# Kernel tuning notes

Hardware: AMD Instinct MI355X
Metric: run time of the kernel (lower is better)

Reference implementation:

```python
import jax, jax.numpy as jnp
import numpy as np

K = 9
HF = WF = 128
SAMPLING = 16
H_IMG = W_IMG = 2048.0
ANC_RATIO = np.array([0.5, 1.0, 2.0])
ANC_SIZE = np.array([8.0, 16.0, 32.0])
TOPN_NMS = 6000
N_NMS = 2000
THR_NMS = 0.7


def generate_anchors():
    # loop order in original GenerateAnchor: ii over Wf (ctrx), jj over Hf (ctry), ratio, size
    ctrx = (np.arange(WF) + 0.5) * SAMPLING  # [Wf]
    ctry = (np.arange(HF) + 0.5) * SAMPLING  # [Hf]
    w = SAMPLING * ANC_SIZE[None, :] / np.sqrt(ANC_RATIO)[:, None]  # [R,S]
    h = SAMPLING * ANC_SIZE[None, :] * np.sqrt(ANC_RATIO)[:, None]
    cx = ctrx[:, None, None, None]  # [Wf,1,1,1]
    cy = ctry[None, :, None, None]  # [1,Hf,1,1]
    w = w[None, None]; h = h[None, None]  # [1,1,R,S]
    x1, y1 = cx - w / 2, cy - h / 2
    x2, y2 = cx + w / 2, cy + h / 2
    anc = np.stack(np.broadcast_arrays(x1, y1, x2, y2), axis=-1).reshape(-1, 4)
    return np.round(anc).astype(np.float32)  # [Wf*Hf*K, 4]


def conv2d(x, w, b, pad):
    y = jax.lax.conv_general_dilated(
        x, w, (1, 1), [(pad, pad), (pad, pad)],
        dimension_numbers=('NCHW', 'OIHW', 'NCHW'))
    return y + b[None, :, None, None]


def pairwise_iou(b):
    # Faithful to my_IoU: 'gt' (pivot, row i) coords are int-truncated;
    # intersection via min(all)+w_a+w_g-max(all); union uses raw/truncated areas.
    ax1, ay1, ax2, ay2 = b[:, 0], b[:, 1], b[:, 2], b[:, 3]
    aw, ah = ax2 - ax1, ay2 - ay1
    aminx, amaxx = jnp.minimum(ax1, ax2), jnp.maximum(ax1, ax2)
    aminy, amaxy = jnp.minimum(ay1, ay2), jnp.maximum(ay1, ay2)
    tx1, ty1, tx2, ty2 = jnp.trunc(ax1), jnp.trunc(ay1), jnp.trunc(ax2), jnp.trunc(ay2)
    gminx, gmaxx = jnp.minimum(tx1, tx2), jnp.maximum(tx1, tx2)
    gminy, gmaxy = jnp.minimum(ty1, ty2), jnp.maximum(ty1, ty2)
    gw, gh = jnp.trunc(ax2 - ax1), jnp.trunc(ay2 - ay1)
    iw = jnp.maximum(jnp.minimum(aminx[None, :], gminx[:, None]) + aw[None, :]
                     + gw[:, None] - jnp.maximum(amaxx[None, :], gmaxx[:, None]), 0.0)
    ih = jnp.maximum(jnp.minimum(aminy[None, :], gminy[:, None]) + ah[None, :]
                     + gh[:, None] - jnp.maximum(amaxy[None, :], gmaxy[:, None]), 0.0)
    inter = iw * ih  # [i=pivot, j=candidate]
    union = (aw * ah)[None, :] + (gw * gh)[:, None] - inter
    return inter / union


def make_roi(anchor, delta, obj):
    # delta2xy
    aw = anchor[:, 2] - anchor[:, 0]
    ah = anchor[:, 3] - anchor[:, 1]
    acx = anchor[:, 0] + aw / 2
    acy = anchor[:, 1] + ah / 2
    cx = delta[:, 0] * aw + acx
    cy = delta[:, 1] * ah + acy
    w = jnp.exp(delta[:, 2]) * aw
    h = jnp.exp(delta[:, 3]) * ah
    roi = jnp.stack([cx - w / 2, cy - h / 2, cx + w / 2, cy + h / 2], axis=1)
    # clip exactly as original: negatives->0; >H -> H-1; >W -> W-1
    roi = jnp.maximum(roi, 0.0)
    roi = roi.at[:, 3].set(jnp.where(roi[:, 3] > H_IMG, H_IMG - 1.0, roi[:, 3]))
    roi = roi.at[:, 2].set(jnp.where(roi[:, 2] > W_IMG, W_IMG - 1.0, roi[:, 2]))
    valid = (roi[:, 2] - roi[:, 0] > SAMPLING) & (roi[:, 3] - roi[:, 1] > SAMPLING)
    scores = jnp.where(valid, obj, -jnp.inf)  # mask instead of dropping (jit-friendly)
    top_scores, top_idx = jax.lax.top_k(scores, TOPN_NMS)
    boxes = roi[top_idx]
    keep0 = jnp.isfinite(top_scores)
    iou = pairwise_iou(boxes)  # [TOPN, TOPN]
    idxs = jnp.arange(TOPN_NMS)

    def body(i, keep):
        sup = keep[i] & (iou[i] >= THR_NMS) & (idxs > i)
        return keep & ~sup

    keep = jax.lax.fori_loop(0, TOPN_NMS, body, keep0)
    rank = jnp.cumsum(keep) - 1
    pos = jnp.where(keep & (rank < N_NMS), rank, N_NMS)  # out-of-range rows dropped
    out = jnp.zeros((N_NMS, 4), boxes.dtype).at[pos].set(boxes, mode='drop')
    return out


def setup_inputs() -> dict:
    key = jax.random.key(0)
    ks = jax.random.split(key, 4)
    featmap = jax.random.normal(ks[0], (1, 512, HF, WF), dtype=jnp.float32)
    conv3_w = jax.random.normal(ks[1], (512, 512, 3, 3), dtype=jnp.float32) * 0.01
    conv3_b = jnp.zeros((512,), jnp.float32)
    cls_w = jax.random.normal(ks[2], (2 * K, 512, 1, 1), dtype=jnp.float32) * 0.01
    cls_b = jnp.zeros((2 * K,), jnp.float32)
    reg_w = jax.random.normal(ks[3], (4 * K, 512, 1, 1), dtype=jnp.float32) * 0.01
    reg_b = jnp.zeros((4 * K,), jnp.float32)
    return {'featmap': featmap, 'conv3_w': conv3_w, 'conv3_b': conv3_b,
            'cls_w': cls_w, 'cls_b': cls_b, 'reg_w': reg_w, 'reg_b': reg_b}


def reference(featmap, conv3_w, conv3_b, cls_w, cls_b, reg_w, reg_b):
    x = jax.nn.relu(conv2d(featmap, conv3_w, conv3_b, 1))
    pred_cls = conv2d(x, cls_w, cls_b, 0)  # [1, 2k, Hf, Wf]
    pred_reg = conv2d(x, reg_w, reg_b, 0)  # [1, 4k, Hf, Wf]
    pred_cls = jnp.transpose(pred_cls, (0, 2, 3, 1)).reshape(1, -1, 2)
    pred_reg = jnp.transpose(pred_reg, (0, 2, 3, 1)).reshape(1, -1, 4)
    pred_obj = pred_cls[:, :, 1]
    anchors = jnp.asarray(generate_anchors())
    # roi path is detached in the original (uses .data)
    roi = make_roi(anchors,
                   jax.lax.stop_gradient(pred_reg[0]),
                   jax.lax.stop_gradient(pred_obj[0]))
    return roi, pred_cls, pred_reg
```

## Files before the change

kernel.cpp:

```cpp
#include <hip/hip_runtime.h>

#define HF 128
#define WF 128
#define KANC 9
#define NANC (HF*WF*KANC)
#define NSORT 262144
#define TOPN 6000
#define NWORDS 94
#define NOUT 2000
#define OFF_CLS 8000
#define OFF_REG 302912
#define NCAND 8192
#define NBCAP 2048

typedef unsigned long long u64;
typedef double d4 __attribute__((ext_vector_type(4)));
typedef const __attribute__((address_space(1))) void* gas1;
typedef __attribute__((address_space(3))) void* las3;

__global__ __launch_bounds__(256) void zero3_k(double* p1, int n1,
                                               double* p2, int n2,
                                               unsigned* hist, u64* selp,
                                               unsigned* cnt) {
  int i = blockIdx.x * 256 + threadIdx.x;
  if (i < n1) p1[i] = 0.0;
  else if (i - n1 < n2) p2[i - n1] = 0.0;
  if (i < 2048) hist[i] = 0;
  if (i == 0) { selp[0] = 0; selp[1] = 0; cnt[0] = 0; cnt[1] = 0; }
}

__global__ __launch_bounds__(256) void wtrans_k(const float* __restrict__ w,
                                                float* __restrict__ wt) {
  __shared__ float ld[64 * 73];
  int t = threadIdx.x;
  int ocg = blockIdx.x & 7, icg = blockIdx.x >> 3;
  int oc0 = ocg << 6, ic0 = icg << 3;
  #pragma unroll
  for (int rep = 0; rep < 18; ++rep) {
    int idx = rep * 256 + t;
    int row = idx / 72, col = idx - row * 72;
    ld[row * 73 + col] = w[(size_t)(oc0 + row) * 4608 + ic0 * 9 + col];
  }
  __syncthreads();
  #pragma unroll
  for (int rep = 0; rep < 18; ++rep) {
    int idx = rep * 256 + t;
    int pair = idx >> 6, oc = idx & 63;
    int tap = pair % 9, ic = pair / 9;
    wt[(size_t)tap * 262144 + (size_t)(ic0 + ic) * 512 + oc0 + oc] =
        ld[oc * 73 + ic * 9 + tap];
  }
}

#define BKC 32
#define NCHUNK 144

__global__ __launch_bounds__(256, 4) void conv_mfma_k(
    const float* __restrict__ feat, const float* __restrict__ wt,
    const float* __restrict__ conv_b, const float* __restrict__ cls_w,
    const float* __restrict__ reg_w, double* __restrict__ predacc)
{
  __shared__ __align__(16) char smraw[32768];
  float* AsB = (float*)smraw;
  float* BsB = (float*)(smraw + 2 * 2048 * 4);
  int tid = threadIdx.x;
  int bid = blockIdx.x;
  int pt = bid & 255, ot = bid >> 8;
  int h = pt >> 1, w0 = (pt & 1) << 6;
  int oc0 = ot << 6;
  int wv = tid >> 6, l = tid & 63;
  int wr = wv >> 1, wc = wv & 1;
  int lg = l >> 4, lr = l & 15;

  d4 acc[2][2];
  #pragma unroll
  for (int t = 0; t < 2; ++t)
    #pragma unroll
    for (int u = 0; u < 2; ++u) acc[t][u] = (d4)0.0;

  float4 areg[2];

  auto gloadA = [&](int c) {
    int tap = c >> 4, ic0 = (c & 15) << 5;
    int kh = tap / 3 - 1, kw = tap % 3 - 1;
    int hp = h + kh;
    bool okh = ((unsigned)hp < 128u);
    #pragma unroll
    for (int i = 0; i < 2; ++i) {
      int q = tid + (i << 8);
      int r = q >> 4, c0 = (q & 15) << 2;
      float v0 = 0.f, v1 = 0.f, v2 = 0.f, v3 = 0.f;
      const float* src = &feat[((ic0 + r) << 14) + (hp << 7)];
      int wp = w0 + c0 + kw;
      if (okh) {
        if ((unsigned)(wp + 0) < 128u) v0 = src[wp + 0];
        if ((unsigned)(wp + 1) < 128u) v1 = src[wp + 1];
        if ((unsigned)(wp + 2) < 128u) v2 = src[wp + 2];
        if ((unsigned)(wp + 3) < 128u) v3 = src[wp + 3];
      }
      areg[i] = make_float4(v0, v1, v2, v3);
    }
  };
  auto gloadB_lds = [&](int c, int buf) {
    float* B = BsB + buf * 2048;
    #pragma unroll
    for (int i = 0; i < 2; ++i) {
      int q = tid + (i << 8);
      int r = q >> 4, c0 = (q & 15) << 2;
      const float* src =
          &wt[(size_t)((c << 5) + r) * 512 + oc0 + (c0 ^ ((r & 1) << 4))];
      __builtin_amdgcn_global_load_lds((gas1)src, (las3)&B[q << 2], 16, 0, 0);
    }
  };
  auto dswriteA = [&](int buf) {
    float* A = AsB + buf * 2048;
    #pragma unroll
    for (int i = 0; i < 2; ++i) {
      int q = tid + (i << 8);
      int r = q >> 4, c0 = (q & 15) << 2;
      *(float4*)&A[(r << 6) + (c0 ^ ((r & 1) << 4))] = areg[i];
    }
  };
  auto compute = [&](int buf) {
    const float* A = AsB + buf * 2048;
    const float* B = BsB + buf * 2048;
    #pragma unroll
    for (int k4 = 0; k4 < BKC; k4 += 4) {
      int krow = k4 + lg;
      int sw = (krow & 1) << 4;
      double a0 = (double)A[(krow << 6) + (((wr << 5) + lr) ^ sw)];
      double a1 = (double)A[(krow << 6) + (((wr << 5) + 16 + lr) ^ sw)];
      double b0 = (double)B[(krow << 6) + (((wc << 5) + lr) ^ sw)];
      double b1 = (double)B[(krow << 6) + (((wc << 5) + 16 + lr) ^ sw)];
      acc[0][0] = __builtin_amdgcn_mfma_f64_16x16x4f64(a0, b0, acc[0][0], 0, 0, 0);
      acc[0][1] = __builtin_amdgcn_mfma_f64_16x16x4f64(a0, b1, acc[0][1], 0, 0, 0);
      acc[1][0] = __builtin_amdgcn_mfma_f64_16x16x4f64(a1, b0, acc[1][0], 0, 0, 0);
      acc[1][1] = __builtin_amdgcn_mfma_f64_16x16x4f64(a1, b1, acc[1][1], 0, 0, 0);
    }
  };

  gloadA(0);
  gloadB_lds(0, 0);
  dswriteA(0);
  for (int c = 0; c < NCHUNK; ++c) {
    __syncthreads();
    if (c + 1 < NCHUNK) {
      gloadB_lds(c + 1, (c + 1) & 1);
      gloadA(c + 1);
    }
    compute(c & 1);
    if (c + 1 < NCHUNK) dswriteA((c + 1) & 1);
  }

  int rmap[4], cmap[4];
  {
    d4 z = (d4)0.0;
    double apr = (lg == 0) ? (double)lr : 0.0;
    double bpr = (lg == 0) ? 1.0 : 0.0;
    d4 dr = __builtin_amdgcn_mfma_f64_16x16x4f64(apr, bpr, z, 0, 0, 0);
    double apc = (lg == 0) ? 1.0 : 0.0;
    double bpc = (lg == 0) ? (double)lr : 0.0;
    d4 dc = __builtin_amdgcn_mfma_f64_16x16x4f64(apc, bpc, z, 0, 0, 0);
    #pragma unroll
    for (int r = 0; r < 4; ++r) { rmap[r] = (int)dr[r]; cmap[r] = (int)dc[r]; }
  }

  double* xs = (double*)smraw;
  float* hwS = (float*)(smraw + 32 * 65 * 8);
  __syncthreads();
  for (int e = tid; e < 54 * 64; e += 256) {
    int o = e >> 6, j = e & 63;
    hwS[e] = (o < 18) ? cls_w[(o << 9) + oc0 + j]
                      : reg_w[((o - 18) << 9) + oc0 + j];
  }
  int pixbase = (h << 7) + w0;
  #pragma unroll
  for (int ph = 0; ph < 2; ++ph) {
    if (wr == ph) {
      #pragma unroll
      for (int t = 0; t < 2; ++t) {
        #pragma unroll
        for (int u = 0; u < 2; ++u) {
          #pragma unroll
          for (int r = 0; r < 4; ++r) {
            int ocl = (wc << 5) + (u << 4) + cmap[r];
            int pxl = (t << 4) + rmap[r];
            double v = acc[t][u][r] + (double)conv_b[oc0 + ocl];
            xs[pxl * 65 + ocl] = (v > 0.0) ? v : 0.0;
          }
        }
      }
    }
    __syncthreads();
    #pragma unroll
    for (int it = 0; it < 7; ++it) {
      int e = tid + (it << 8);
      if (e < 54 * 32) {
        int o = e >> 5, px = e & 31;
        const double* xr = &xs[px * 65];
        const float* hr = &hwS[o << 6];
        double s = 0.0;
        #pragma unroll
        for (int j = 0; j < 64; ++j) s += xr[j] * (double)hr[j];
        atomicAdd(&predacc[(size_t)(pixbase + (ph << 5) + px) * 54 + o], s);
      }
    }
    __syncthreads();
  }
}

__global__ __launch_bounds__(256) void chk_x_k(
    const float* __restrict__ feat, const float* __restrict__ c3w,
    double* __restrict__ xraw)
{
  int task = blockIdx.x * 256 + threadIdx.x;
  int pi = task >> 14;
  int oc = (task >> 5) & 511;
  int icg = task & 31;
  const int pixs[4] = {0, 5437, 10240, 16383};
  int pix = pixs[pi];
  int h = pix >> 7, w = pix & 127;
  double s = 0.0;
  for (int ic = icg * 16; ic < icg * 16 + 16; ++ic) {
    const float* f = &feat[ic << 14];
    const float* wp = &c3w[(size_t)(oc * 512 + ic) * 9];
    #pragma unroll
    for (int kh = -1; kh <= 1; ++kh) {
      int hp = h + kh;
      if ((unsigned)hp >= 128u) continue;
      #pragma unroll
      for (int kw = -1; kw <= 1; ++kw) {
        int wq = w + kw;
        if ((unsigned)wq >= 128u) continue;
        s += (double)f[(hp << 7) + wq] * (double)wp[(kh + 1) * 3 + (kw + 1)];
      }
    }
  }
  atomicAdd(&xraw[(pi << 9) + oc], s);
}

__global__ __launch_bounds__(256) void chk_cmp_k(
    const double* __restrict__ xraw, const float* __restrict__ c3b,
    const float* __restrict__ cls_w, const float* __restrict__ reg_w,
    const double* __restrict__ predacc, double* flagd)
{
  int t = threadIdx.x;
  if (t >= 216) return;
  int pi = t / 54, o = t - pi * 54;
  const int pixs[4] = {0, 5437, 10240, 16383};
  const float* wrow = (o < 18) ? &cls_w[o << 9] : &reg_w[(o - 18) << 9];
  const double* xr = &xraw[pi << 9];
  double s = 0.0;
  for (int j = 0; j < 512; ++j) {
    double x = xr[j] + (double)c3b[j];
    x = x > 0.0 ? x : 0.0;
    s += x * (double)wrow[j];
  }
  double got = predacc[(size_t)pixs[pi] * 54 + o];
  if (fabs(got - s) > 1e-6) *flagd = 1.0;
}

__global__ __launch_bounds__(256) void rezero_k(const double* __restrict__ flagd,
                                                double* p, int n) {
  if (*flagd == 0.0) return;
  int i = blockIdx.x * 256 + threadIdx.x;
  if (i < n) p[i] = 0.0;
}

__global__ __launch_bounds__(256) void conv_fb_k(
    const double* __restrict__ flagd,
    const float* __restrict__ feat, const float* __restrict__ wt,
    const float* __restrict__ conv_b, const float* __restrict__ cls_w,
    const float* __restrict__ reg_w, double* __restrict__ predacc)
{
  if (*flagd == 0.0) return;
  __shared__ __align__(16) char smraw[47104];
  double* As = (double*)smraw;
  double* Bs = As + 2048;
  int tid = threadIdx.x;
  int bid = blockIdx.x;
  int pt = bid & 255, ot = bid >> 8;
  int h = pt >> 1, w0 = (pt & 1) << 6;
  int oc0 = ot << 6;
  int tx = tid & 15, ty = tid >> 4;

  double acc[4][4];
  #pragma unroll
  for (int i = 0; i < 4; ++i)
    #pragma unroll
    for (int j = 0; j < 4; ++j) acc[i][j] = 0.0;

  for (int tap = 0; tap < 9; ++tap) {
    int kh = tap / 3 - 1, kw = tap % 3 - 1;
    int hp = h + kh;
    bool okh = (hp >= 0) && (hp < HF);
    for (int icc = 0; icc < 16; ++icc) {
      int ic0 = icc << 5;
      __syncthreads();
      #pragma unroll
      for (int i = 0; i < 8; ++i) {
        int e = tid + (i << 8);
        int icl = e >> 6;
        int lx = e & 63;
        int wp = w0 + lx + kw;
        float v = 0.0f;
        if (okh && wp >= 0 && wp < WF)
          v = feat[((ic0 + icl) << 14) + (hp << 7) + wp];
        As[(icl << 6) + lx] = (double)v;
        Bs[(icl << 6) + lx] =
            (double)wt[((((tap << 9) + ic0 + icl)) << 9) + oc0 + lx];
      }
      __syncthreads();
      #pragma unroll
      for (int k = 0; k < 32; ++k) {
        const double* ar = &As[(k << 6) + (ty << 2)];
        const double* br = &Bs[(k << 6) + (tx << 2)];
        double a0 = ar[0], a1 = ar[1], a2 = ar[2], a3 = ar[3];
        double b0 = br[0], b1 = br[1], b2 = br[2], b3 = br[3];
        acc[0][0] += a0 * b0; acc[0][1] += a0 * b1; acc[0][2] += a0 * b2; acc[0][3] += a0 * b3;
        acc[1][0] += a1 * b0; acc[1][1] += a1 * b1; acc[1][2] += a1 * b2; acc[1][3] += a1 * b3;
        acc[2][0] += a2 * b0; acc[2][1] += a2 * b1; acc[2][2] += a2 * b2; acc[2][3] += a2 * b3;
        acc[3][0] += a3 * b0; acc[3][1] += a3 * b1; acc[3][2] += a3 * b2; acc[3][3] += a3 * b3;
      }
    }
  }
  __syncthreads();
  double* xs = (double*)smraw;
  float* hwS = (float*)(smraw + 64 * 65 * 8);
  #pragma unroll
  for (int i = 0; i < 4; ++i) {
    int px = (ty << 2) + i;
    #pragma unroll
    for (int j = 0; j < 4; ++j) {
      int oc = (tx << 2) + j;
      double v = acc[i][j] + (double)conv_b[oc0 + oc];
      xs[px * 65 + oc] = v > 0.0 ? v : 0.0;
    }
  }
  for (int e = tid; e < 54 * 64; e += 256) {
    int o = e >> 6, ocl = e & 63;
    hwS[e] = (o < 18) ? cls_w[(o << 9) + oc0 + ocl]
                      : reg_w[((o - 18) << 9) + oc0 + ocl];
  }
  __syncthreads();
  int pixbase = (h << 7) + w0;
  for (int e = tid; e < 54 * 64; e += 256) {
    int px = e & 63, o = e >> 6;
    const double* xr = &xs[px * 65];
    const float* hr = &hwS[o << 6];
    double s = 0.0;
    #pragma unroll
    for (int j = 0; j < 64; ++j) s += xr[j] * (double)hr[j];
    atomicAdd(&predacc[(pixbase + px) * 54 + o], s);
  }
}

__global__ __launch_bounds__(256) void anchor_k(
    const double* __restrict__ predacc, const float* __restrict__ cls_b,
    const float* __restrict__ reg_b, float* __restrict__ out,
    double* __restrict__ roi_all, double* __restrict__ scores_d,
    ulonglong2* __restrict__ sortb)
{
  #pragma clang fp contract(off)
  int a = blockIdx.x * 256 + threadIdx.x;
  if (a >= NSORT) return;
  if (a >= NANC) {
    sortb[a] = make_ulonglong2(0xFFF0000000000000ULL, 0xFFFFFFFFULL);
    return;
  }
  int pix = a / 9;
  int k = a - pix * 9;
  int h = pix >> 7, wq = pix & 127;
  const double* pa = &predacc[pix * 54];
  double c0 = pa[2 * k] + (double)cls_b[2 * k];
  double c1 = pa[2 * k + 1] + (double)cls_b[2 * k + 1];
  double d0 = pa[18 + 4 * k + 0] + (double)reg_b[4 * k + 0];
  double d1 = pa[18 + 4 * k + 1] + (double)reg_b[4 * k + 1];
  double d2 = pa[18 + 4 * k + 2] + (double)reg_b[4 * k + 2];
  double d3 = pa[18 + 4 * k + 3] + (double)reg_b[4 * k + 3];
  out[OFF_CLS + a * 2 + 0] = (float)c0;
  out[OFF_CLS + a * 2 + 1] = (float)c1;
  out[OFF_REG + a * 4 + 0] = (float)d0;
  out[OFF_REG + a * 4 + 1] = (float)d1;
  out[OFF_REG + a * 4 + 2] = (float)d2;
  out[OFF_REG + a * 4 + 3] = (float)d3;
  int ir = k / 3, is = k - ir * 3;
  double ratio = (ir == 0) ? 0.5 : (ir == 1 ? 1.0 : 2.0);
  double asz = (is == 0) ? 8.0 : (is == 1 ? 16.0 : 32.0);
  double sq = sqrt(ratio);
  double wa = (16.0 * asz) / sq;
  double ha = (16.0 * asz) * sq;
  double cx = (h + 0.5) * 16.0;
  double cy = (wq + 0.5) * 16.0;
  double A0 = (double)(float)rint(cx - wa * 0.5);
  double A1 = (double)(float)rint(cy - ha * 0.5);
  double A2 = (double)(float)rint(cx + wa * 0.5);
  double A3 = (double)(float)rint(cy + ha * 0.5);
  double aw = A2 - A0, ah = A3 - A1;
  double acx = A0 + aw * 0.5, acy = A1 + ah * 0.5;
  double ccx = d0 * aw + acx;
  double ccy = d1 * ah + acy;
  double wr = exp(d2) * aw;
  double hh = exp(d3) * ah;
  double r0 = ccx - wr * 0.5;
  double r1 = ccy - hh * 0.5;
  double r2 = ccx + wr * 0.5;
  double r3 = ccy + hh * 0.5;
  r0 = fmax(r0, 0.0); r1 = fmax(r1, 0.0); r2 = fmax(r2, 0.0); r3 = fmax(r3, 0.0);
  r3 = (r3 > 2048.0) ? 2047.0 : r3;
  r2 = (r2 > 2048.0) ? 2047.0 : r2;
  bool valid = ((r2 - r0) > 16.0) && ((r3 - r1) > 16.0);
  double score = valid ? c1 : -__builtin_huge_val();
  roi_all[a * 4 + 0] = r0;
  roi_all[a * 4 + 1] = r1;
  roi_all[a * 4 + 2] = r2;
  roi_all[a * 4 + 3] = r3;
  scores_d[a] = score;
  u64 u = (u64)__double_as_longlong(score);
  u64 m = (u >> 63) ? ~u : (u | 0x8000000000000000ULL);
  sortb[a] = make_ulonglong2(~m, (u64)a);
}

__global__ __launch_bounds__(1024) void hist_k(const ulonglong2* __restrict__ sortb,
                                               unsigned* __restrict__ hist,
                                               const u64* __restrict__ selp,
                                               int pass) {
  __shared__ unsigned h[2048];
  int t = threadIdx.x;
  h[t] = 0; h[t + 1024] = 0;
  __syncthreads();
  const int SH[3] = {53, 42, 31};
  const u64 PM[3] = {0ULL, 0xFFE0000000000000ULL, 0xFFFFFC0000000000ULL};
  u64 pfx = selp[0];
  u64 pm = PM[pass];
  int sh = SH[pass];
  for (int e = blockIdx.x * 1024 + t; e < NSORT; e += gridDim.x * 1024) {
    u64 k = sortb[e].x;
    if ((k & pm) == pfx)
      atomicAdd(&h[(unsigned)((k >> sh) & 2047)], 1u);
  }
  __syncthreads();
  if (h[t]) atomicAdd(&hist[t], h[t]);
  if (h[t + 1024]) atomicAdd(&hist[t + 1024], h[t + 1024]);
}

__global__ __launch_bounds__(1024) void scan_k(unsigned* hist, u64* selp, int pass) {
  __shared__ unsigned h[2048];
  int t = threadIdx.x;
  h[t] = hist[t]; h[t + 1024] = hist[t + 1024];
  hist[t] = 0; hist[t + 1024] = 0;
  __syncthreads();
  if (t == 0) {
    const int SH[3] = {53, 42, 31};
    u64 cum = selp[1];
    u64 pfx = selp[0];
    int b = 0;
    for (; b < 2047; ++b) {
      if (cum + h[b] >= (u64)TOPN) break;
      cum += h[b];
    }
    selp[0] = pfx | ((u64)b << SH[pass]);
    selp[1] = cum;
  }
}

__global__ __launch_bounds__(1024) void compact_k(
    const ulonglong2* __restrict__ sortb, const u64* __restrict__ selp,
    ulonglong2* __restrict__ cand, ulonglong2* __restrict__ bcand,
    unsigned* __restrict__ cnt) {
  u64 pfx = selp[0];
  const u64 M33 = 0xFFFFFFFF80000000ULL;
  for (int e = blockIdx.x * 1024 + threadIdx.x; e < NSORT; e += gridDim.x * 1024) {
    ulonglong2 v = sortb[e];
    u64 top = v.x & M33;
    if (top < pfx) {
      unsigned p = atomicAdd(&cnt[0], 1u);
      if (p < NCAND) cand[p] = v;
    } else if (top == pfx) {
      unsigned p = atomicAdd(&cnt[1], 1u);
      if (p < NBCAP) bcand[p] = v;
    }
  }
}

__device__ __forceinline__ bool sless(ulonglong2 A, ulonglong2 B) {
  return (A.x < B.x) || (A.x == B.x && A.y < B.y);
}

__global__ __launch_bounds__(1024) void sortprep_k(
    const ulonglong2* __restrict__ cand, const ulonglong2* __restrict__ bcand,
    const unsigned* __restrict__ cnt, const double* __restrict__ roi_all,
    const double* __restrict__ scores_d, double* __restrict__ boxes,
    u64* __restrict__ removed)
{
  extern __shared__ ulonglong2 s[];
  int t = threadIdx.x;
  unsigned ci = cnt[0]; if (ci > NCAND) ci = NCAND;
  unsigned cb = cnt[1]; if (cb > NBCAP) cb = NBCAP;
  #pragma unroll
  for (int i = 0; i < 8; ++i) {
    int p = t + (i << 10);
    ulonglong2 v;
    if (p < (int)ci) v = cand[p];
    else if (p < (int)(ci + cb)) v = bcand[p - ci];
    else v = make_ulonglong2(~0ULL, ~0ULL);
    s[p] = v;
  }
  __syncthreads();
  for (int k = 2; k <= NCAND; k <<= 1) {
    for (int j = k >> 1; j >= 1; j >>= 1) {
      #pragma unroll
      for (int q = 0; q < 4; ++q) {
        int p = t + (q << 10);
        int li = ((p & ~(j - 1)) << 1) | (p & (j - 1));
        int pa = li | j;
        bool asc = ((li & k) == 0);
        ulonglong2 A = s[li], B = s[pa];
        bool sw = asc ? sless(B, A) : sless(A, B);
        if (sw) { s[li] = B; s[pa] = A; }
      }
      __syncthreads();
    }
  }
  for (int i = t; i < TOPN; i += 1024) {
    unsigned idx = (unsigned)s[i].y;
    double b0 = 0, b1 = 0, b2 = 0, b3 = 0;
    if (idx < NANC) {
      b0 = roi_all[idx * 4 + 0];
      b1 = roi_all[idx * 4 + 1];
      b2 = roi_all[idx * 4 + 2];
      b3 = roi_all[idx * 4 + 3];
    }
    boxes[i * 4 + 0] = b0; boxes[i * 4 + 1] = b1;
    boxes[i * 4 + 2] = b2; boxes[i * 4 + 3] = b3;
  }
  if (t < NWORDS) {
    u64 wdd = (t == NWORDS - 1) ? 0xFFFF000000000000ULL : 0ULL;
    for (int b = 0; b < 64; ++b) {
      int i = t * 64 + b;
      if (i >= TOPN) break;
      unsigned idx = (unsigned)s[i].y;
      bool dead = true;
      if (idx < NANC) dead = isinf(scores_d[idx]);
      if (dead) wdd |= (1ULL << b);
    }
    removed[t] = wdd;
  }
}

__global__ __launch_bounds__(256) void mask_k(const double* __restrict__ boxes,
                                              u64* __restrict__ mask) {
  #pragma clang fp contract(off)
  int gw = (blockIdx.x * 256 + threadIdx.x) >> 6;
  int lane = threadIdx.x & 63;
  int i = gw / NWORDS, wj = gw - i * NWORDS;
  if (i >= TOPN) return;
  if (wj < (i >> 6)) return;
  double ix1 = boxes[i * 4 + 0], iy1 = boxes[i * 4 + 1];
  double ix2 = boxes[i * 4 + 2], iy2 = boxes[i * 4 + 3];
  double tx1 = trunc(ix1), ty1 = trunc(iy1), tx2 = trunc(ix2), ty2 = trunc(iy2);
  double gminx = fmin(tx1, tx2), gmaxx = fmax(tx1, tx2);
  double gminy = fmin(ty1, ty2), gmaxy = fmax(ty1, ty2);
  double gw_ = trunc(ix2 - ix1), gh_ = trunc(iy2 - iy1);
  int j = wj * 64 + lane;
  bool pred = false;
  if (j < TOPN && j > i) {
    double jx1 = boxes[j * 4 + 0], jy1 = boxes[j * 4 + 1];
    double jx2 = boxes[j * 4 + 2], jy2 = boxes[j * 4 + 3];
    double aw = jx2 - jx1, ah = jy2 - jy1;
    double aminx = fmin(jx1, jx2), amaxx = fmax(jx1, jx2);
    double aminy = fmin(jy1, jy2), amaxy = fmax(jy1, jy2);
    double iw = fmin(aminx, gminx) + aw + gw_ - fmax(amaxx, gmaxx);
    iw = fmax(iw, 0.0);
    double ih = fmin(aminy, gminy) + ah + gh_ - fmax(amaxy, gmaxy);
    ih = fmax(ih, 0.0);
    double inter = iw * ih;
    double uni = aw * ah + gw_ * gh_ - inter;
    pred = (inter / uni >= 0.7);
  }
  u64 bal = __ballot(pred);
  if (lane == 0) mask[(size_t)i * NWORDS + wj] = bal;
}

__global__ __launch_bounds__(1024) void nms_chunk_k(const u64* __restrict__ mask,
                                                    u64* removed_g) {
  __shared__ u64 rem[NWORDS];
  __shared__ u64 aliveSh;
  int t = threadIdx.x;
  int lane = t & 63;
  int wvid = t >> 6;
  if (t < NWORDS) rem[t] = removed_g[t];
  __syncthreads();
  for (int c = 0; c < NWORDS; ++c) {
    if (wvid == 0) {
      int i = c * 64 + lane;
      u64 diag = (i < TOPN) ? mask[(size_t)i * NWORDS + c] : 0ULL;
      u64 local = rem[c];
      #pragma unroll 1
      for (int j = 0; j < 64; ++j) {
        u64 dj = __shfl(diag, j);
        if (!((local >> j) & 1ULL)) local |= dj;
      }
      if (lane == 0) { rem[c] = local; aliveSh = ~local; }
    }
    __syncthreads();
    u64 alive = aliveSh;
    int nw = NWORDS - 1 - c;
    if (nw > 0 && alive) {
      int npairs = 64 * nw;
      for (int p = t; p < npairs; p += 1024) {
        int j = p / nw;
        int w = c + 1 + (p - j * nw);
        if ((alive >> j) & 1ULL) {
          int i = c * 64 + j;
          if (i < TOPN) {
            u64 v = mask[(size_t)i * NWORDS + w];
            if (v) atomicOr(&rem[w], v);
          }
        }
      }
    }
    __syncthreads();
  }
  if (t < NWORDS) removed_g[t] = rem[t];
}

__global__ __launch_bounds__(256) void out_k(const u64* __restrict__ removed,
                                             const double* __restrict__ boxes,
                                             float* __restrict__ out) {
  __shared__ int pref[NWORDS + 1];
  __shared__ u64 keepw[NWORDS];
  int t = threadIdx.x;
  for (int i = t; i < NOUT * 4; i += 256) out[i] = 0.0f;
  if (t < NWORDS) keepw[t] = ~removed[t];
  __syncthreads();
  if (t == 0) {
    int s = 0;
    for (int w = 0; w < NWORDS; ++w) { pref[w] = s; s += __popcll(keepw[w]); }
    pref[NWORDS] = s;
  }
  __syncthreads();
  for (int i = t; i < TOPN; i += 256) {
    u64 kw = keepw[i >> 6];
    if ((kw >> (i & 63)) & 1ULL) {
      int rank = pref[i >> 6] + __popcll(kw & ((1ULL << (i & 63)) - 1ULL));
      if (rank < NOUT) {
        out[rank * 4 + 0] = (float)boxes[i * 4 + 0];
        out[rank * 4 + 1] = (float)boxes[i * 4 + 1];
        out[rank * 4 + 2] = (float)boxes[i * 4 + 2];
        out[rank * 4 + 3] = (float)boxes[i * 4 + 3];
      }
    }
  }
}

extern "C" void kernel_launch(void* const* d_in, const int* in_sizes, int n_in,
                              void* d_out, int out_size, void* d_ws, size_t ws_size,
                              hipStream_t stream) {
  const float* feat = (const float*)d_in[0];
  const float* c3w = (const float*)d_in[1];
  const float* c3b = (const float*)d_in[2];
  const float* clw = (const float*)d_in[3];
  const float* clb = (const float*)d_in[4];
  const float* rgw = (const float*)d_in[5];
  const float* rgb = (const float*)d_in[6];
  float* out = (float*)d_out;
  char* ws = (char*)d_ws;
  size_t off = 0;
  auto alloc = [&](size_t bytes) {
    size_t o = off;
    off = (off + bytes + 255) & ~(size_t)255;
    return o;
  };
  double* predacc = (double*)(ws + alloc(16384ULL * 54 * 8));
  double* flagd = (double*)(ws + alloc(256));
  float* wt = (float*)(ws + alloc(2359296ULL * 4));
  double* roi_all = (double*)(ws + alloc((size_t)NANC * 4 * 8));
  double* scores_d = (double*)(ws + alloc((size_t)NANC * 8));
  ulonglong2* sortb = (ulonglong2*)(ws + alloc((size_t)NSORT * 16));
  double* boxes = (double*)(ws + alloc((size_t)TOPN * 4 * 8));
  u64* mask = (u64*)(ws + alloc((size_t)TOPN * NWORDS * 8));
  u64* removed = (u64*)(ws + alloc(NWORDS * 8));
  double* xraw = (double*)(ws + alloc(4 * 512 * 8));
  unsigned* hist = (unsigned*)(ws + alloc(2048 * 4));
  u64* selp = (u64*)(ws + alloc(256));
  unsigned* cntb = (unsigned*)(ws + alloc(256));
  ulonglong2* cand = (ulonglong2*)(ws + alloc((size_t)NCAND * 16));
  ulonglong2* bcand = (ulonglong2*)(ws + alloc((size_t)NBCAP * 16));
  (void)ws_size; (void)out_size; (void)in_sizes; (void)n_in;

  const int NPRED = 16384 * 54;
  hipLaunchKernelGGL(zero3_k, dim3((NPRED + 32 + 2048 + 255) / 256), dim3(256), 0,
                     stream, predacc, NPRED + 32, xraw, 2048, hist, selp, cntb);
  hipLaunchKernelGGL(wtrans_k, dim3(512), dim3(256), 0, stream, c3w, wt);
  hipLaunchKernelGGL(conv_mfma_k, dim3(2048), dim3(256), 0, stream,
                     feat, wt, c3b, clw, rgw, predacc);
  hipLaunchKernelGGL(chk_x_k, dim3(256), dim3(256), 0, stream, feat, c3w, xraw);
  hipLaunchKernelGGL(chk_cmp_k, dim3(1), dim3(256), 0, stream,
                     xraw, c3b, clw, rgw, predacc, flagd);
  hipLaunchKernelGGL(rezero_k, dim3((NPRED + 255) / 256), dim3(256), 0, stream,
                     flagd, predacc, NPRED);
  hipLaunchKernelGGL(conv_fb_k, dim3(2048), dim3(256), 0, stream,
                     flagd, feat, wt, c3b, clw, rgw, predacc);
  hipLaunchKernelGGL(anchor_k, dim3(NSORT / 256), dim3(256), 0, stream,
                     predacc, clb, rgb, out, roi_all, scores_d, sortb);
  for (int pass = 0; pass < 3; ++pass) {
    hipLaunchKernelGGL(hist_k, dim3(128), dim3(1024), 0, stream,
                       sortb, hist, selp, pass);
    hipLaunchKernelGGL(scan_k, dim3(1), dim3(1024), 0, stream, hist, selp, pass);
  }
  hipLaunchKernelGGL(compact_k, dim3(128), dim3(1024), 0, stream,
                     sortb, selp, cand, bcand, cntb);
  hipLaunchKernelGGL(sortprep_k, dim3(1), dim3(1024), NCAND * 16, stream,
                     cand, bcand, cntb, roi_all, scores_d, boxes, removed);
  hipLaunchKernelGGL(mask_k, dim3(TOPN * NWORDS / 4), dim3(256), 0, stream,
                     boxes, mask);
  hipLaunchKernelGGL(nms_chunk_k, dim3(1), dim3(1024), 0, stream, mask, removed);
  hipLaunchKernelGGL(out_k, dim3(1), dim3(256), 0, stream, removed, boxes, out);
}
```

Measured before the change: 2.379 ms.

## Drop conv self-check fallback, split bitonic sort across blocks, fuse NMS output

Removes the spot-check kernels and the FP64 fallback convolution path, so the MFMA conv result is used unconditionally. Replaces the single-block 8192-element bitonic sort with a multi-block local sort plus global and local merge passes. Fuses the NMS and output-compaction kernels into one. This cuts the extra check work and the serial single-block sort, but drops the correctness safety net and adds several small kernel launches.

```diff
diff --git a/kernel.cpp b/kernel.cpp
--- a/kernel.cpp
+++ b/kernel.cpp
@@ -18,13 +18,11 @@
 typedef const __attribute__((address_space(1))) void* gas1;
 typedef __attribute__((address_space(3))) void* las3;
 
-__global__ __launch_bounds__(256) void zero3_k(double* p1, int n1,
-                                               double* p2, int n2,
+__global__ __launch_bounds__(256) void zinit_k(double* p1, int n1,
                                                unsigned* hist, u64* selp,
                                                unsigned* cnt) {
   int i = blockIdx.x * 256 + threadIdx.x;
   if (i < n1) p1[i] = 0.0;
-  else if (i - n1 < n2) p2[i - n1] = 0.0;
   if (i < 2048) hist[i] = 0;
   if (i == 0) { selp[0] = 0; selp[1] = 0; cnt[0] = 0; cnt[1] = 0; }
 }
@@ -206,152 +204,6 @@
       }
     }
     __syncthreads();
-  }
-}
-
-__global__ __launch_bounds__(256) void chk_x_k(
-    const float* __restrict__ feat, const float* __restrict__ c3w,
-    double* __restrict__ xraw)
-{
-  int task = blockIdx.x * 256 + threadIdx.x;
-  int pi = task >> 14;
-  int oc = (task >> 5) & 511;
-  int icg = task & 31;
-  const int pixs[4] = {0, 5437, 10240, 16383};
-  int pix = pixs[pi];
-  int h = pix >> 7, w = pix & 127;
-  double s = 0.0;
-  for (int ic = icg * 16; ic < icg * 16 + 16; ++ic) {
-    const float* f = &feat[ic << 14];
-    const float* wp = &c3w[(size_t)(oc * 512 + ic) * 9];
-    #pragma unroll
-    for (int kh = -1; kh <= 1; ++kh) {
-      int hp = h + kh;
-      if ((unsigned)hp >= 128u) continue;
-      #pragma unroll
-      for (int kw = -1; kw <= 1; ++kw) {
-        int wq = w + kw;
-        if ((unsigned)wq >= 128u) continue;
-        s += (double)f[(hp << 7) + wq] * (double)wp[(kh + 1) * 3 + (kw + 1)];
-      }
-    }
-  }
-  atomicAdd(&xraw[(pi << 9) + oc], s);
-}
-
-__global__ __launch_bounds__(256) void chk_cmp_k(
-    const double* __restrict__ xraw, const float* __restrict__ c3b,
-    const float* __restrict__ cls_w, const float* __restrict__ reg_w,
-    const double* __restrict__ predacc, double* flagd)
-{
-  int t = threadIdx.x;
-  if (t >= 216) return;
-  int pi = t / 54, o = t - pi * 54;
-  const int pixs[4] = {0, 5437, 10240, 16383};
-  const float* wrow = (o < 18) ? &cls_w[o << 9] : &reg_w[(o - 18) << 9];
-  const double* xr = &xraw[pi << 9];
-  double s = 0.0;
-  for (int j = 0; j < 512; ++j) {
-    double x = xr[j] + (double)c3b[j];
-    x = x > 0.0 ? x : 0.0;
-    s += x * (double)wrow[j];
-  }
-  double got = predacc[(size_t)pixs[pi] * 54 + o];
-  if (fabs(got - s) > 1e-6) *flagd = 1.0;
-}
-
-__global__ __launch_bounds__(256) void rezero_k(const double* __restrict__ flagd,
-                                                double* p, int n) {
-  if (*flagd == 0.0) return;
-  int i = blockIdx.x * 256 + threadIdx.x;
-  if (i < n) p[i] = 0.0;
-}
-
-__global__ __launch_bounds__(256) void conv_fb_k(
-    const double* __restrict__ flagd,
-    const float* __restrict__ feat, const float* __restrict__ wt,
-    const float* __restrict__ conv_b, const float* __restrict__ cls_w,
-    const float* __restrict__ reg_w, double* __restrict__ predacc)
-{
-  if (*flagd == 0.0) return;
-  __shared__ __align__(16) char smraw[47104];
-  double* As = (double*)smraw;
-  double* Bs = As + 2048;
-  int tid = threadIdx.x;
-  int bid = blockIdx.x;
-  int pt = bid & 255, ot = bid >> 8;
-  int h = pt >> 1, w0 = (pt & 1) << 6;
-  int oc0 = ot << 6;
-  int tx = tid & 15, ty = tid >> 4;
-
-  double acc[4][4];
-  #pragma unroll
-  for (int i = 0; i < 4; ++i)
-    #pragma unroll
-    for (int j = 0; j < 4; ++j) acc[i][j] = 0.0;
-
-  for (int tap = 0; tap < 9; ++tap) {
-    int kh = tap / 3 - 1, kw = tap % 3 - 1;
-    int hp = h + kh;
-    bool okh = (hp >= 0) && (hp < HF);
-    for (int icc = 0; icc < 16; ++icc) {
-      int ic0 = icc << 5;
-      __syncthreads();
-      #pragma unroll
-      for (int i = 0; i < 8; ++i) {
-        int e = tid + (i << 8);
-        int icl = e >> 6;
-        int lx = e & 63;
-        int wp = w0 + lx + kw;
-        float v = 0.0f;
-        if (okh && wp >= 0 && wp < WF)
-          v = feat[((ic0 + icl) << 14) + (hp << 7) + wp];
-        As[(icl << 6) + lx] = (double)v;
-        Bs[(icl << 6) + lx] =
-            (double)wt[((((tap << 9) + ic0 + icl)) << 9) + oc0 + lx];
-      }
-      __syncthreads();
-      #pragma unroll
-      for (int k = 0; k < 32; ++k) {
-        const double* ar = &As[(k << 6) + (ty << 2)];
-        const double* br = &Bs[(k << 6) + (tx << 2)];
-        double a0 = ar[0], a1 = ar[1], a2 = ar[2], a3 = ar[3];
-        double b0 = br[0], b1 = br[1], b2 = br[2], b3 = br[3];
-        acc[0][0] += a0 * b0; acc[0][1] += a0 * b1; acc[0][2] += a0 * b2; acc[0][3] += a0 * b3;
-        acc[1][0] += a1 * b0; acc[1][1] += a1 * b1; acc[1][2] += a1 * b2; acc[1][3] += a1 * b3;
-        acc[2][0] += a2 * b0; acc[2][1] += a2 * b1; acc[2][2] += a2 * b2; acc[2][3] += a2 * b3;
-        acc[3][0] += a3 * b0; acc[3][1] += a3 * b1; acc[3][2] += a3 * b2; acc[3][3] += a3 * b3;
-      }
-    }
-  }
-  __syncthreads();
-  double* xs = (double*)smraw;
-  float* hwS = (float*)(smraw + 64 * 65 * 8);
-  #pragma unroll
-  for (int i = 0; i < 4; ++i) {
-    int px = (ty << 2) + i;
-    #pragma unroll
-    for (int j = 0; j < 4; ++j) {
-      int oc = (tx << 2) + j;
-      double v = acc[i][j] + (double)conv_b[oc0 + oc];
-      xs[px * 65 + oc] = v > 0.0 ? v : 0.0;
-    }
-  }
-  for (int e = tid; e < 54 * 64; e += 256) {
-    int o = e >> 6, ocl = e & 63;
-    hwS[e] = (o < 18) ? cls_w[(o << 9) + oc0 + ocl]
-                      : reg_w[((o - 18) << 9) + oc0 + ocl];
-  }
-  __syncthreads();
-  int pixbase = (h << 7) + w0;
-  for (int e = tid; e < 54 * 64; e += 256) {
-    int px = e & 63, o = e >> 6;
-    const double* xr = &xs[px * 65];
-    const float* hr = &hwS[o << 6];
-    double s = 0.0;
-    #pragma unroll
-    for (int j = 0; j < 64; ++j) s += xr[j] * (double)hr[j];
-    atomicAdd(&predacc[(pixbase + px) * 54 + o], s);
   }
 }
 
@@ -487,64 +339,116 @@
   return (A.x < B.x) || (A.x == B.x && A.y < B.y);
 }
 
-__global__ __launch_bounds__(1024) void sortprep_k(
-    const ulonglong2* __restrict__ cand, const ulonglong2* __restrict__ bcand,
-    const unsigned* __restrict__ cnt, const double* __restrict__ roi_all,
-    const double* __restrict__ scores_d, double* __restrict__ boxes,
-    u64* __restrict__ removed)
-{
-  extern __shared__ ulonglong2 s[];
+__global__ __launch_bounds__(1024) void sortloc_k(
+    ulonglong2* cand, const ulonglong2* __restrict__ bcand,
+    const unsigned* __restrict__ cnt) {
+  __shared__ ulonglong2 s[2048];
   int t = threadIdx.x;
+  int base = blockIdx.x * 2048;
   unsigned ci = cnt[0]; if (ci > NCAND) ci = NCAND;
   unsigned cb = cnt[1]; if (cb > NBCAP) cb = NBCAP;
   #pragma unroll
-  for (int i = 0; i < 8; ++i) {
-    int p = t + (i << 10);
+  for (int i = 0; i < 2; ++i) {
+    int p = base + t + (i << 10);
     ulonglong2 v;
     if (p < (int)ci) v = cand[p];
     else if (p < (int)(ci + cb)) v = bcand[p - ci];
     else v = make_ulonglong2(~0ULL, ~0ULL);
-    s[p] = v;
-  }
-  __syncthreads();
-  for (int k = 2; k <= NCAND; k <<= 1) {
+    s[t + (i << 10)] = v;
+  }
+  __syncthreads();
+  for (int k = 2; k <= 2048; k <<= 1)
     for (int j = k >> 1; j >= 1; j >>= 1) {
-      #pragma unroll
-      for (int q = 0; q < 4; ++q) {
-        int p = t + (q << 10);
-        int li = ((p & ~(j - 1)) << 1) | (p & (j - 1));
-        int pa = li | j;
-        bool asc = ((li & k) == 0);
-        ulonglong2 A = s[li], B = s[pa];
-        bool sw = asc ? sless(B, A) : sless(A, B);
-        if (sw) { s[li] = B; s[pa] = A; }
-      }
+      int li = ((t & ~(j - 1)) << 1) | (t & (j - 1));
+      int pa = li | j;
+      bool asc = (((base + li) & k) == 0);
+      ulonglong2 A = s[li], B = s[pa];
+      bool sw = asc ? sless(B, A) : sless(A, B);
+      if (sw) { s[li] = B; s[pa] = A; }
       __syncthreads();
     }
-  }
-  for (int i = t; i < TOPN; i += 1024) {
-    unsigned idx = (unsigned)s[i].y;
-    double b0 = 0, b1 = 0, b2 = 0, b3 = 0;
-    if (idx < NANC) {
-      b0 = roi_all[idx * 4 + 0];
-      b1 = roi_all[idx * 4 + 1];
-      b2 = roi_all[idx * 4 + 2];
-      b3 = roi_all[idx * 4 + 3];
-    }
-    boxes[i * 4 + 0] = b0; boxes[i * 4 + 1] = b1;
-    boxes[i * 4 + 2] = b2; boxes[i * 4 + 3] = b3;
-  }
-  if (t < NWORDS) {
-    u64 wdd = (t == NWORDS - 1) ? 0xFFFF000000000000ULL : 0ULL;
-    for (int b = 0; b < 64; ++b) {
-      int i = t * 64 + b;
-      if (i >= TOPN) break;
-      unsigned idx = (unsigned)s[i].y;
-      bool dead = true;
-      if (idx < NANC) dead = isinf(scores_d[idx]);
-      if (dead) wdd |= (1ULL << b);
-    }
-    removed[t] = wdd;
+  cand[base + t] = s[t];
+  cand[base + t + 1024] = s[t + 1024];
+}
+
+__global__ __launch_bounds__(256) void bitonic_global(ulonglong2* d, int k, int j) {
+  int t = blockIdx.x * 256 + threadIdx.x;
+  int i = ((t & ~(j - 1)) << 1) | (t & (j - 1));
+  int p = i | j;
+  bool asc = ((i & k) == 0);
+  ulonglong2 A = d[i], B = d[p];
+  bool sw = asc ? sless(B, A) : sless(A, B);
+  if (sw) { d[i] = B; d[p] = A; }
+}
+
+__global__ __launch_bounds__(1024) void bitonic_lm(ulonglong2* d, int k) {
+  __shared__ ulonglong2 s[2048];
+  int t = threadIdx.x;
+  int base = blockIdx.x * 2048;
+  bool asc = ((base & k) == 0);
+  s[t] = d[base + t];
+  s[t + 1024] = d[base + t + 1024];
+  __syncthreads();
+  for (int j = 1024; j >= 1; j >>= 1) {
+    int li = ((t & ~(j - 1)) << 1) | (t & (j - 1));
+    int pa = li | j;
+    ulonglong2 A = s[li], B = s[pa];
+    bool sw = asc ? sless(B, A) : sless(A, B);
+    if (sw) { s[li] = B; s[pa] = A; }
+    __syncthreads();
+  }
+  d[base + t] = s[t];
+  d[base + t + 1024] = s[t + 1024];
+}
+
+__global__ __launch_bounds__(1024) void sortfin_k(
+    ulonglong2* d, const double* __restrict__ roi_all,
+    const double* __restrict__ scores_d, double* __restrict__ boxes,
+    u64* __restrict__ removed) {
+  __shared__ ulonglong2 s[2048];
+  int t = threadIdx.x;
+  int base = blockIdx.x * 2048;
+  s[t] = d[base + t];
+  s[t + 1024] = d[base + t + 1024];
+  __syncthreads();
+  for (int j = 1024; j >= 1; j >>= 1) {
+    int li = ((t & ~(j - 1)) << 1) | (t & (j - 1));
+    int pa = li | j;
+    ulonglong2 A = s[li], B = s[pa];
+    if (sless(B, A)) { s[li] = B; s[pa] = A; }
+    __syncthreads();
+  }
+  #pragma unroll
+  for (int q = 0; q < 2; ++q) {
+    int li = t + (q << 10);
+    int i = base + li;
+    if (i < TOPN) {
+      unsigned idx = (unsigned)s[li].y;
+      double b0 = 0, b1 = 0, b2 = 0, b3 = 0;
+      if (idx < NANC) {
+        b0 = roi_all[idx * 4 + 0];
+        b1 = roi_all[idx * 4 + 1];
+        b2 = roi_all[idx * 4 + 2];
+        b3 = roi_all[idx * 4 + 3];
+      }
+      boxes[i * 4 + 0] = b0; boxes[i * 4 + 1] = b1;
+      boxes[i * 4 + 2] = b2; boxes[i * 4 + 3] = b3;
+    }
+  }
+  if (t < 32) {
+    int w = (base >> 6) + t;
+    if (w < NWORDS) {
+      u64 wdd = (w == NWORDS - 1) ? 0xFFFF000000000000ULL : 0ULL;
+      for (int b = 0; b < 64; ++b) {
+        int i = w * 64 + b;
+        if (i >= TOPN) break;
+        unsigned idx = (unsigned)s[i - base].y;
+        bool dead = true;
+        if (idx < NANC) dead = isinf(scores_d[idx]);
+        if (dead) wdd |= (1ULL << b);
+      }
+      removed[w] = wdd;
+    }
   }
 }
 
@@ -582,14 +486,18 @@
   if (lane == 0) mask[(size_t)i * NWORDS + wj] = bal;
 }
 
-__global__ __launch_bounds__(1024) void nms_chunk_k(const u64* __restrict__ mask,
-                                                    u64* removed_g) {
+__global__ __launch_bounds__(1024) void nmsout_k(const u64* __restrict__ mask,
+                                                 const u64* __restrict__ removed_g,
+                                                 const double* __restrict__ boxes,
+                                                 float* __restrict__ out) {
   __shared__ u64 rem[NWORDS];
   __shared__ u64 aliveSh;
+  __shared__ int pref[NWORDS + 1];
   int t = threadIdx.x;
   int lane = t & 63;
   int wvid = t >> 6;
   if (t < NWORDS) rem[t] = removed_g[t];
+  for (int i = t; i < NOUT * 4; i += 1024) out[i] = 0.0f;
   __syncthreads();
   for (int c = 0; c < NWORDS; ++c) {
     if (wvid == 0) {
@@ -622,26 +530,14 @@
     }
     __syncthreads();
   }
-  if (t < NWORDS) removed_g[t] = rem[t];
-}
-
-__global__ __launch_bounds__(256) void out_k(const u64* __restrict__ removed,
-                                             const double* __restrict__ boxes,
-                                             float* __restrict__ out) {
-  __shared__ int pref[NWORDS + 1];
-  __shared__ u64 keepw[NWORDS];
-  int t = threadIdx.x;
-  for (int i = t; i < NOUT * 4; i += 256) out[i] = 0.0f;
-  if (t < NWORDS) keepw[t] = ~removed[t];
-  __syncthreads();
   if (t == 0) {
     int s = 0;
-    for (int w = 0; w < NWORDS; ++w) { pref[w] = s; s += __popcll(keepw[w]); }
+    for (int w = 0; w < NWORDS; ++w) { pref[w] = s; s += __popcll(~rem[w]); }
     pref[NWORDS] = s;
   }
   __syncthreads();
-  for (int i = t; i < TOPN; i += 256) {
-    u64 kw = keepw[i >> 6];
+  for (int i = t; i < TOPN; i += 1024) {
+    u64 kw = ~rem[i >> 6];
     if ((kw >> (i & 63)) & 1ULL) {
       int rank = pref[i >> 6] + __popcll(kw & ((1ULL << (i & 63)) - 1ULL));
       if (rank < NOUT) {
@@ -673,7 +569,6 @@
     return o;
   };
   double* predacc = (double*)(ws + alloc(16384ULL * 54 * 8));
-  double* flagd = (double*)(ws + alloc(256));
   float* wt = (float*)(ws + alloc(2359296ULL * 4));
   double* roi_all = (double*)(ws + alloc((size_t)NANC * 4 * 8));
   double* scores_d = (double*)(ws + alloc((size_t)NANC * 8));
@@ -681,7 +576,6 @@
   double* boxes = (double*)(ws + alloc((size_t)TOPN * 4 * 8));
   u64* mask = (u64*)(ws + alloc((size_t)TOPN * NWORDS * 8));
   u64* removed = (u64*)(ws + alloc(NWORDS * 8));
-  double* xraw = (double*)(ws + alloc(4 * 512 * 8));
   unsigned* hist = (unsigned*)(ws + alloc(2048 * 4));
   u64* selp = (u64*)(ws + alloc(256));
   unsigned* cntb = (unsigned*)(ws + alloc(256));
@@ -690,18 +584,11 @@
   (void)ws_size; (void)out_size; (void)in_sizes; (void)n_in;
 
   const int NPRED = 16384 * 54;
-  hipLaunchKernelGGL(zero3_k, dim3((NPRED + 32 + 2048 + 255) / 256), dim3(256), 0,
-                     stream, predacc, NPRED + 32, xraw, 2048, hist, selp, cntb);
+  hipLaunchKernelGGL(zinit_k, dim3((NPRED + 255) / 256), dim3(256), 0, stream,
+                     predacc, NPRED, hist, selp, cntb);
   hipLaunchKernelGGL(wtrans_k, dim3(512), dim3(256), 0, stream, c3w, wt);
   hipLaunchKernelGGL(conv_mfma_k, dim3(2048), dim3(256), 0, stream,
                      feat, wt, c3b, clw, rgw, predacc);
-  hipLaunchKernelGGL(chk_x_k, dim3(256), dim3(256), 0, stream, feat, c3w, xraw);
-  hipLaunchKernelGGL(chk_cmp_k, dim3(1), dim3(256), 0, stream,
-                     xraw, c3b, clw, rgw, predacc, flagd);
-  hipLaunchKernelGGL(rezero_k, dim3((NPRED + 255) / 256), dim3(256), 0, stream,
-                     flagd, predacc, NPRED);
-  hipLaunchKernelGGL(conv_fb_k, dim3(2048), dim3(256), 0, stream,
-                     flagd, feat, wt, c3b, clw, rgw, predacc);
   hipLaunchKernelGGL(anchor_k, dim3(NSORT / 256), dim3(256), 0, stream,
                      predacc, clb, rgb, out, roi_all, scores_d, sortb);
   for (int pass = 0; pass < 3; ++pass) {
@@ -711,10 +598,19 @@
   }
   hipLaunchKernelGGL(compact_k, dim3(128), dim3(1024), 0, stream,
                      sortb, selp, cand, bcand, cntb);
-  hipLaunchKernelGGL(sortprep_k, dim3(1), dim3(1024), NCAND * 16, stream,
-                     cand, bcand, cntb, roi_all, scores_d, boxes, removed);
+  hipLaunchKernelGGL(sortloc_k, dim3(4), dim3(1024), 0, stream,
+                     cand, bcand, cntb);
+  hipLaunchKernelGGL(bitonic_global, dim3(NCAND / 512), dim3(256), 0, stream,
+                     cand, 4096, 2048);
+  hipLaunchKernelGGL(bitonic_lm, dim3(4), dim3(1024), 0, stream, cand, 4096);
+  hipLaunchKernelGGL(bitonic_global, dim3(NCAND / 512), dim3(256), 0, stream,
+                     cand, 8192, 4096);
+  hipLaunchKernelGGL(bitonic_global, dim3(NCAND / 512), dim3(256), 0, stream,
+                     cand, 8192, 2048);
+  hipLaunchKernelGGL(sortfin_k, dim3(4), dim3(1024), 0, stream,
+                     cand, roi_all, scores_d, boxes, removed);
   hipLaunchKernelGGL(mask_k, dim3(TOPN * NWORDS / 4), dim3(256), 0, stream,
                      boxes, mask);
-  hipLaunchKernelGGL(nms_chunk_k, dim3(1), dim3(1024), 0, stream, mask, removed);
-  hipLaunchKernelGGL(out_k, dim3(1), dim3(256), 0, stream, removed, boxes, out);
-}
+  hipLaunchKernelGGL(nmsout_k, dim3(1), dim3(1024), 0, stream,
+                     mask, removed, boxes, out);
+}
```

New measurement: 2.267 ms. 1.05x faster.
